# Kernel optimization log

Measured on AMD Instinct MI355X. Metric: run time of the kernel, lower is better.

Reference implementation:

```python
import jax, jax.numpy as jnp
import numpy as np

TOP_K = 48
NUM_RBF = 16
NUM_RBF_SC = 8
MAXREL = 32
EDGE_F = 128
EPS_D = 1e-6
LN_EPS = 1e-5


def gather_nodes(nodes, idx):
    # nodes: [B, L, C], idx: [B, L, K] -> [B, L, K, C]
    return jax.vmap(lambda n, i: n[i])(nodes, idx)


def rbf(D, count):
    # D: [..., ] -> [..., count]; mu in [2, 22], sigma = 20/count
    mu = jnp.linspace(2.0, 22.0, count)
    sigma = (22.0 - 2.0) / count
    return jnp.exp(-(((D[..., None] - mu) / sigma) ** 2))


def layer_norm(x, g, b):
    mu = jnp.mean(x, -1, keepdims=True)
    var = jnp.mean((x - mu) ** 2, -1, keepdims=True)
    return g * (x - mu) / jnp.sqrt(var + LN_EPS) + b


def setup_inputs() -> dict:
    key = jax.random.key(0)
    ks = jax.random.split(key, 8)
    B, Lr = 1, 1024
    X = jax.random.normal(ks[0], (B, Lr, 37, 3), dtype=jnp.float32)
    mask = jnp.ones((B, Lr), dtype=jnp.float32)
    atom_mask = jnp.ones((B, Lr, 37), dtype=jnp.float32)
    residue_idx = jnp.arange(B * Lr, dtype=jnp.int64 if jax.config.jax_enable_x64 else jnp.int32).reshape(B, Lr)
    dihedral_mask = jnp.ones((B, Lr), dtype=jnp.float32)
    chain_labels = jnp.zeros((B, Lr), dtype=jnp.int32)
    W_pos = jax.random.normal(ks[1], (16, 2 * MAXREL + 2), dtype=jnp.float32) * 0.1
    b_pos = jnp.zeros((16,), dtype=jnp.float32)
    W_e = jax.random.normal(ks[2], (EDGE_F, 16 + NUM_RBF * 25), dtype=jnp.float32) * 0.05
    g_e = jnp.ones((EDGE_F,), dtype=jnp.float32)
    be_e = jnp.zeros((EDGE_F,), dtype=jnp.float32)
    W_s = jax.random.normal(ks[3], (EDGE_F, NUM_RBF_SC * 32 * 5), dtype=jnp.float32) * 0.05
    g_s = jnp.ones((EDGE_F,), dtype=jnp.float32)
    b_s = jnp.zeros((EDGE_F,), dtype=jnp.float32)
    return {"X": X, "L": 1024, "mask": mask, "atom_mask": atom_mask,
            "residue_idx": residue_idx, "dihedral_mask": dihedral_mask,
            "chain_labels": chain_labels, "W_pos": W_pos, "b_pos": b_pos,
            "W_e": W_e, "g_e": g_e, "be_e": be_e, "W_s": W_s, "g_s": g_s, "b_s": b_s}


def reference(X, L, mask, atom_mask, residue_idx, dihedral_mask, chain_labels,
              W_pos, b_pos, W_e, g_e, be_e, W_s, g_s, b_s):
    # Virtual Cb from ideal geometry
    b_v = X[:, :, 1, :] - X[:, :, 0, :]
    c_v = X[:, :, 2, :] - X[:, :, 1, :]
    a_v = jnp.cross(b_v, c_v)
    Cb = -0.58273431 * a_v + 0.56802827 * b_v - 0.54067466 * c_v + X[:, :, 1, :]
    Ca = X[:, :, 1, :]
    N = X[:, :, 0, :]
    C = X[:, :, 2, :]
    O = X[:, :, 4, :]

    # _dist: masked pairwise Ca distances + top-k smallest
    mask2d = mask[:, None, :] * mask[:, :, None]  # [B, L, L]
    dX = Ca[:, :, None, :] - Ca[:, None, :, :]
    D = mask2d * jnp.sqrt(jnp.sum(dX ** 2, -1) + EPS_D)
    D_max = jnp.max(D, -1, keepdims=True)
    D_adj = D + (1.0 - mask2d) * D_max
    neg_vals, E_idx = jax.lax.top_k(-D_adj, TOP_K)
    D_neighbors = -neg_vals  # [B, L, K]

    coords = {'N': N, 'Ca': Ca, 'C': C, 'O': O, 'Cb': Cb}
    pairs = [('N','N'),('C','C'),('O','O'),('Cb','Cb'),('Ca','N'),('Ca','C'),('Ca','O'),
             ('Ca','Cb'),('N','C'),('N','O'),('N','Cb'),('Cb','C'),('Cb','O'),('O','C'),
             ('N','Ca'),('C','Ca'),('O','Ca'),('Cb','Ca'),('C','N'),('O','N'),('Cb','N'),
             ('C','Cb'),('O','Cb'),('C','O')]
    A_st = jnp.stack([coords[a] for a, _ in pairs])  # [24, B, L, 3]
    B_st = jnp.stack([coords[b] for _, b in pairs])
    B_nb = jax.vmap(gather_nodes, (0, None))(B_st, E_idx)  # [24, B, L, K, 3]
    Dp = jnp.sqrt(jnp.sum((A_st[:, :, :, None, :] - B_nb) ** 2, -1) + EPS_D)  # [24,B,L,K]
    RBF_pairs = rbf(Dp, NUM_RBF)  # [24, B, L, K, 16]
    Bt, Lr, K = E_idx.shape
    RBF_pairs = jnp.moveaxis(RBF_pairs, 0, 3).reshape(Bt, Lr, K, 24 * NUM_RBF)
    RBF_all = jnp.concatenate([rbf(D_neighbors, NUM_RBF), RBF_pairs], -1)  # [B,L,K,400]

    # Positional encodings
    ri_nb = gather_nodes(residue_idx[..., None], E_idx)[..., 0]  # [B,L,K]
    offset = residue_idx[:, :, None] - ri_nb
    ch_nb = gather_nodes(chain_labels[..., None], E_idx)[..., 0]
    E_chains = (chain_labels[:, :, None] - ch_nb == 0).astype(jnp.int32)
    d = jnp.clip(offset + MAXREL, 0, 2 * MAXREL) * E_chains + (1 - E_chains) * (2 * MAXREL + 1)
    d_onehot = jax.nn.one_hot(d, 2 * MAXREL + 2, dtype=jnp.float32)
    E_positional = d_onehot @ W_pos.T + b_pos
    E = jnp.concatenate([E_positional, RBF_all], -1)  # [B,L,K,416]

    # Sidechain RBFs on the first min(100, K) neighbors
    Ks = min(100, K)
    E_idx_sub = E_idx[:, :, :Ks]
    am_g = gather_nodes(atom_mask, E_idx_sub)  # [B,L,Ks,37]
    S = X[:, :, 5:37, :]  # [B,L,32,3]
    S_nb = gather_nodes(S.reshape(Bt, Lr, 32 * 3), E_idx_sub).reshape(Bt, Lr, Ks, 32, 3)
    anchors = jnp.stack([N, Ca, C, O, Cb], 2)  # [B,L,5,3], anchor order matches loop order
    Ds = jnp.sqrt(jnp.sum((anchors[:, :, None, :, None, :] - S_nb[:, :, :, None, :, :]) ** 2, -1) + EPS_D)
    # Ds: [B,L,Ks,5,32]; rbf_side -> [B,L,Ks,5,32,8]; masked by neighbor atom mask
    RBF_s = rbf(Ds, NUM_RBF_SC) * am_g[:, :, :, None, 5:37, None]
    E_s = RBF_s.reshape(Bt, Lr, Ks, 5 * 32 * NUM_RBF_SC)  # [B,L,Ks,1280]

    E_s = layer_norm(E_s @ W_s.T, g_s, b_s)
    E = layer_norm(E @ W_e.T, g_e, be_e)
    return (E, E_idx, E_s, E_idx_sub)
```

## Files before the change

### kernel.cpp

```cpp
#include <hip/hip_runtime.h>
#include <math.h>

#define LRES 1024
#define TOPK 48
#define NEDGE (LRES*TOPK)

typedef short short8 __attribute__((ext_vector_type(8)));
typedef float f32x4  __attribute__((ext_vector_type(4)));

#define OUT_E     0
#define OUT_EIDX  6291456
#define OUT_ES    6340608
#define OUT_EIDX2 12632064

#define WS_COORDS 0
#define WS_DNB    15360
#define WS_EIDX   64512
#define WS_WPE    113664
#define WS_WPS    140288

#define DE 1.06666667f
#define QE 0.10273976f
#define DS 1.14285714f
#define QS 0.07337053f

__constant__ int PA[24] = {0,2,3,4,1,1,1,1,0,0,0,4,4,3,0,2,3,4,2,3,4,2,3,2};
__constant__ int PB[24] = {0,2,3,4,0,2,3,4,2,3,4,2,3,2,1,1,1,1,0,0,0,4,4,3};

__device__ inline short f2bf(float f) {
    unsigned u = __float_as_uint(f);
    unsigned r = (u + 0x7FFFu + ((u >> 16) & 1u)) >> 16;
    return (short)r;
}

__device__ inline short8 pack8(const float* fv) {
    union { short8 s; unsigned u[4]; } r;
    #pragma unroll
    for (int i = 0; i < 4; ++i)
        r.u[i] = __builtin_amdgcn_perm(__float_as_uint(fv[2*i+1]),
                                       __float_as_uint(fv[2*i]), 0x07060302u);
    return r.s;
}

__global__ __launch_bounds__(256) void k_pre(const float* __restrict__ X,
                                             const float* __restrict__ mask,
                                             const float* __restrict__ We,
                                             const float* __restrict__ Ws,
                                             float* __restrict__ coords,
                                             short* __restrict__ WpE,
                                             short* __restrict__ WpS,
                                             float* __restrict__ Dnb,
                                             int* __restrict__ Eidx,
                                             float* __restrict__ out) {
    int blk = blockIdx.x, t = threadIdx.x;
    if (blk < 256) {
        __shared__ float sCa[LRES*3];
        __shared__ float sM[LRES];
        for (int j = t; j < LRES; j += 256) {
            sCa[j*3+0] = X[j*111 + 3];
            sCa[j*3+1] = X[j*111 + 4];
            sCa[j*3+2] = X[j*111 + 5];
            sM[j] = mask[j];
        }
        __syncthreads();
        int w = t >> 6, lane = t & 63;
        int i = blk * 4 + w;
        float cx = sCa[i*3], cy = sCa[i*3+1], cz = sCa[i*3+2];
        float mi = sM[i];
        float dv[16], m2v[16];
        float lmax = -1e30f;
        #pragma unroll
        for (int s = 0; s < 16; ++s) {
            int j = s*64 + lane;
            float dx = cx - sCa[j*3], dy = cy - sCa[j*3+1], dz = cz - sCa[j*3+2];
            float d  = __builtin_amdgcn_sqrtf(dx*dx + dy*dy + dz*dz + 1e-6f);
            float m2 = mi * sM[j];
            dv[s] = m2 * d; m2v[s] = m2;
            lmax = fmaxf(lmax, dv[s]);
        }
        #pragma unroll
        for (int off = 32; off; off >>= 1) lmax = fmaxf(lmax, __shfl_xor(lmax, off));
        unsigned long long key[16];
        unsigned long long mkey = ~0ull; int mslot = 0;
        #pragma unroll
        for (int s = 0; s < 16; ++s) {
            float dadj = dv[s] + (1.0f - m2v[s]) * lmax;
            key[s] = (((unsigned long long)__float_as_uint(dadj)) << 10) | (unsigned)(s*64 + lane);
            if (key[s] < mkey) { mkey = key[s]; mslot = s; }
        }
        for (int it = 0; it < TOPK; ++it) {
            unsigned long long wk = mkey;
            #pragma unroll
            for (int off = 32; off; off >>= 1) {
                unsigned long long o = __shfl_xor(wk, off);
                wk = (o < wk) ? o : wk;
            }
            if (lane == 0) {
                int j = (int)(wk & 1023u);
                int id = i*TOPK + it;
                Dnb[id]  = __uint_as_float((unsigned)(wk >> 10));
                Eidx[id] = j;
                out[OUT_EIDX  + id] = (float)j;
                out[OUT_EIDX2 + id] = (float)j;
            }
            if (mkey == wk) {
                key[mslot] = ~0ull;
                mkey = ~0ull;
                #pragma unroll
                for (int s = 0; s < 16; ++s)
                    if (key[s] < mkey) { mkey = key[s]; mslot = s; }
            }
        }
    } else if (blk < 896) {
        int g = (blk - 256) * 256 + t;
        if (g < 8*13*64*8) {
            int j = g & 7, lane = (g >> 3) & 63, gg = g >> 9;
            int ks = gg % 13, nt = gg / 13;
            int n = nt*16 + (lane & 15), k = ks*32 + (lane >> 4)*8 + j;
            WpE[g] = f2bf(We[n*416 + k]);
        }
        if (g < 8*40*64*8) {
            int j = g & 7, lane = (g >> 3) & 63, gg = g >> 9;
            int ks = gg % 40, nt = gg / 40;
            int n = nt*16 + (lane & 15), k = ks*32 + (lane >> 4)*8 + j;
            WpS[g] = f2bf(Ws[n*1280 + k]);
        }
    } else {
        int r = (blk - 896) * 256 + t;
        if (r >= LRES) return;
        const float* xr = X + r * 111;
        float N[3], Ca[3], C[3], O[3], bv[3], cv[3], av[3];
        #pragma unroll
        for (int d = 0; d < 3; ++d) {
            N[d]  = xr[0*3 + d];  Ca[d] = xr[1*3 + d];
            C[d]  = xr[2*3 + d];  O[d]  = xr[4*3 + d];
            bv[d] = Ca[d] - N[d]; cv[d] = C[d] - Ca[d];
        }
        av[0] = bv[1]*cv[2] - bv[2]*cv[1];
        av[1] = bv[2]*cv[0] - bv[0]*cv[2];
        av[2] = bv[0]*cv[1] - bv[1]*cv[0];
        float* o = coords + r * 15;
        #pragma unroll
        for (int d = 0; d < 3; ++d) {
            float Cb = -0.58273431f*av[d] + 0.56802827f*bv[d] - 0.54067466f*cv[d] + Ca[d];
            o[0*3+d] = N[d]; o[1*3+d] = Ca[d]; o[2*3+d] = C[d];
            o[3*3+d] = O[d]; o[4*3+d] = Cb;
        }
    }
}

__global__ __launch_bounds__(256, 2) void k_edge(const float* __restrict__ coords,
                                                 const float* __restrict__ X,
                                                 const float* __restrict__ amask,
                                                 const short* __restrict__ WpE,
                                                 const short* __restrict__ WpS,
                                                 const float* __restrict__ Dnb,
                                                 const int* __restrict__ Eidx,
                                                 const int* __restrict__ ri,
                                                 const int* __restrict__ ch,
                                                 const float* __restrict__ Wpos,
                                                 const float* __restrict__ bpos,
                                                 const float* __restrict__ ge,
                                                 const float* __restrict__ be,
                                                 const float* __restrict__ gs,
                                                 const float* __restrict__ bs,
                                                 float* __restrict__ out) {
    __shared__ float smem[5808];
    int t = threadIdx.x;
    int w = t >> 6, lane = t & 63, quad = lane >> 4, l16 = lane & 15;

    if (blockIdx.x < 1536) {
        float* u_hbuf = smem;
        float* sA3    = smem + 4224;
        float* part   = smem + 4272;
        float* part2  = smem + 4528;
        float* smu    = smem + 4784;
        float* srs    = smem + 4816;
        int id0 = blockIdx.x * 32;
        int i0 = id0 / TOPK;

        if (t < 45) {
            int rr = i0 + t / 15;
            if (rr > LRES-1) rr = LRES-1;
            sA3[t] = coords[rr*15 + t%15];
        }
        int s1 = 4*w + quad;
        float S[2][2][3], am[2][2];
        int im[2];
        #pragma unroll
        for (int mt = 0; mt < 2; ++mt) {
            int id = id0 + mt*16 + l16;
            int j  = Eidx[id];
            im[mt] = id / TOPK;
            const float* xp = X + (j*37 + 5)*3;
            const float* ap = amask + j*37 + 5;
            #pragma unroll
            for (int h = 0; h < 2; ++h) {
                int s = s1 + h*16;
                S[mt][h][0] = xp[s*3+0];
                S[mt][h][1] = xp[s*3+1];
                S[mt][h][2] = xp[s*3+2];
                am[mt][h]   = ap[s];
            }
        }
        __syncthreads();

        f32x4 acc[2][8] = {};
        const short8* bp = (const short8*)WpS;

        for (int a = 0; a < 5; ++a) {
            float A[2][3];
            #pragma unroll
            for (int mt = 0; mt < 2; ++mt) {
                int base = (im[mt] - i0)*15 + a*3;
                A[mt][0] = sA3[base+0];
                A[mt][1] = sA3[base+1];
                A[mt][2] = sA3[base+2];
            }
            #pragma unroll
            for (int h = 0; h < 2; ++h) {
                int ks = a*8 + w + h*4;
                short8 afrag[2];
                #pragma unroll
                for (int mt = 0; mt < 2; ++mt) {
                    float dx = A[mt][0] - S[mt][h][0];
                    float dy = A[mt][1] - S[mt][h][1];
                    float dz = A[mt][2] - S[mt][h][2];
                    float d  = __builtin_amdgcn_sqrtf(fmaf(dz,dz,fmaf(dy,dy,fmaf(dx,dx,1e-6f))));
                    float u  = fmaf(d, 0.4f, -0.8f);
                    float e0 = __expf(-u*u) * am[mt][h];
                    float g  = __expf(fmaf(2.0f*DS, u, -DS*DS));
                    float fv[8];
                    fv[0] = e0;
                    #pragma unroll
                    for (int r = 1; r < 8; ++r) { e0 *= g; g *= QS; fv[r] = e0; }
                    afrag[mt] = pack8(fv);
                }
                #pragma unroll
                for (int nt = 0; nt < 8; ++nt) {
                    short8 b = bp[(nt*40 + ks)*64 + lane];
                    acc[0][nt] = __builtin_amdgcn_mfma_f32_16x16x32_bf16(afrag[0], b, acc[0][nt], 0,0,0);
                    acc[1][nt] = __builtin_amdgcn_mfma_f32_16x16x32_bf16(afrag[1], b, acc[1][nt], 0,0,0);
                }
            }
        }

        float* hbuf = u_hbuf;
        __syncthreads();
        for (int ww = 0; ww < 4; ++ww) {
            if (w == ww) {
                #pragma unroll
                for (int mt = 0; mt < 2; ++mt)
                #pragma unroll
                for (int nt = 0; nt < 8; ++nt)
                #pragma unroll
                for (int r = 0; r < 4; ++r) {
                    int e = mt*16 + quad*4 + r;
                    float* p = &hbuf[e*132 + nt*16 + l16];
                    if (ww == 0) *p = acc[mt][nt][r]; else *p += acc[mt][nt][r];
                }
            }
            __syncthreads();
        }
        {
            int e = t >> 3, p = t & 7;
            float s = 0.f, s2 = 0.f;
            #pragma unroll
            for (int q = 0; q < 16; ++q) {
                float x = hbuf[e*132 + p*16 + q];
                s += x; s2 += x*x;
            }
            part[e*8+p] = s; part2[e*8+p] = s2;
        }
        __syncthreads();
        if (t < 32) {
            float s = 0.f, s2 = 0.f;
            #pragma unroll
            for (int p = 0; p < 8; ++p) { s += part[t*8+p]; s2 += part2[t*8+p]; }
            float mu = s * (1.0f/128.0f);
            float var = s2 * (1.0f/128.0f) - mu*mu;
            smu[t] = mu; srs[t] = rsqrtf(var + 1e-5f);
        }
        __syncthreads();
        for (int it = t; it < 32*128; it += 256) {
            int e = it >> 7, f = it & 127;
            float x = hbuf[e*132 + f];
            out[OUT_ES + (size_t)(id0 + e)*128 + f] = gs[f] * (x - smu[e]) * srs[e] + bs[f];
        }
    } else {
        float* sA     = smem;
        float* sB     = smem + 480;
        float* u_hbuf = smem + 960;
        float* part   = smem + 5184;
        float* part2  = smem + 5440;
        float* smu    = smem + 5696;
        float* srs    = smem + 5728;
        int*   sdpos  = (int*)(smem + 5760);
        float* sdist  = u_hbuf;
        float* sposf  = u_hbuf + 32*27;
        int id0 = (blockIdx.x - 1536) * 32;

        if (t < 32) {
            int id = id0 + t, i = id / TOPK, j = Eidx[id];
            int off = ri[i] - ri[j];
            sdpos[t] = (ch[i] == ch[j]) ? min(max(off + 32, 0), 64) : 65;
            sdist[t*27] = Dnb[id];
        }
        for (int it = t; it < 32*15; it += 256) {
            int e = it / 15, q = it % 15;
            int id = id0 + e, i = id / TOPK, j = Eidx[id];
            sA[e*15+q] = coords[i*15+q];
            sB[e*15+q] = coords[j*15+q];
        }
        __syncthreads();
        for (int it = t; it < 32*24; it += 256) {
            int e = it / 24, p = it % 24, a = PA[p], b = PB[p];
            float dx = sA[e*15+a*3+0] - sB[e*15+b*3+0];
            float dy = sA[e*15+a*3+1] - sB[e*15+b*3+1];
            float dz = sA[e*15+a*3+2] - sB[e*15+b*3+2];
            sdist[e*27 + 1 + p] = __builtin_amdgcn_sqrtf(dx*dx + dy*dy + dz*dz + 1e-6f);
        }
        for (int it = t; it < 32*16; it += 256) {
            int e = it >> 4, c = it & 15;
            sposf[e*17 + c] = Wpos[c*66 + sdpos[e]] + bpos[c];
        }
        __syncthreads();

        f32x4 acc[2][8] = {};
        const short8* bp = (const short8*)WpE;
        float rb = (quad & 1) ? 8.0f*DE : 0.0f;

        for (int ks = w; ks < 13; ks += 4) {
            short8 afrag[2];
            #pragma unroll
            for (int mt = 0; mt < 2; ++mt) {
                int e = mt*16 + l16;
                float fv[8];
                if (ks == 0 && quad < 2) {
                    #pragma unroll
                    for (int j = 0; j < 8; ++j) fv[j] = sposf[e*17 + quad*8 + j];
                } else {
                    int p = (ks == 0) ? 0 : (2*ks - 1 + (quad >> 1));
                    float d = sdist[e*27 + p];
                    float u = fmaf(d, 0.8f, -1.6f) - rb;
                    float e0 = __expf(-u*u);
                    float g  = __expf(fmaf(2.0f*DE, u, -DE*DE));
                    fv[0] = e0;
                    #pragma unroll
                    for (int r = 1; r < 8; ++r) { e0 *= g; g *= QE; fv[r] = e0; }
                }
                afrag[mt] = pack8(fv);
            }
            #pragma unroll
            for (int nt = 0; nt < 8; ++nt) {
                short8 b = bp[(nt*13 + ks)*64 + lane];
                acc[0][nt] = __builtin_amdgcn_mfma_f32_16x16x32_bf16(afrag[0], b, acc[0][nt], 0,0,0);
                acc[1][nt] = __builtin_amdgcn_mfma_f32_16x16x32_bf16(afrag[1], b, acc[1][nt], 0,0,0);
            }
        }

        float* hbuf = u_hbuf;
        __syncthreads();
        for (int ww = 0; ww < 4; ++ww) {
            if (w == ww) {
                #pragma unroll
                for (int mt = 0; mt < 2; ++mt)
                #pragma unroll
                for (int nt = 0; nt < 8; ++nt)
                #pragma unroll
                for (int r = 0; r < 4; ++r) {
                    int e = mt*16 + quad*4 + r;
                    float* p = &hbuf[e*132 + nt*16 + l16];
                    if (ww == 0) *p = acc[mt][nt][r]; else *p += acc[mt][nt][r];
                }
            }
            __syncthreads();
        }
        {
            int e = t >> 3, p = t & 7;
            float s = 0.f, s2 = 0.f;
            #pragma unroll
            for (int q = 0; q < 16; ++q) {
                float x = hbuf[e*132 + p*16 + q];
                s += x; s2 += x*x;
            }
            part[e*8+p] = s; part2[e*8+p] = s2;
        }
        __syncthreads();
        if (t < 32) {
            float s = 0.f, s2 = 0.f;
            #pragma unroll
            for (int p = 0; p < 8; ++p) { s += part[t*8+p]; s2 += part2[t*8+p]; }
            float mu = s * (1.0f/128.0f);
            float var = s2 * (1.0f/128.0f) - mu*mu;
            smu[t] = mu; srs[t] = rsqrtf(var + 1e-5f);
        }
        __syncthreads();
        for (int it = t; it < 32*128; it += 256) {
            int e = it >> 7, f = it & 127;
            float x = hbuf[e*132 + f];
            out[OUT_E + (size_t)(id0 + e)*128 + f] = ge[f] * (x - smu[e]) * srs[e] + be[f];
        }
    }
}

extern "C" void kernel_launch(void* const* d_in, const int* in_sizes, int n_in,
                              void* d_out, int out_size, void* d_ws, size_t ws_size,
                              hipStream_t stream) {
    (void)in_sizes; (void)n_in; (void)out_size; (void)ws_size;
    const float* X     = (const float*)d_in[0];
    const float* mask  = (const float*)d_in[2];
    const float* amask = (const float*)d_in[3];
    const int*   ri    = (const int*)d_in[4];
    const int*   ch    = (const int*)d_in[6];
    const float* Wpos  = (const float*)d_in[7];
    const float* bpos  = (const float*)d_in[8];
    const float* We    = (const float*)d_in[9];
    const float* ge    = (const float*)d_in[10];
    const float* be    = (const float*)d_in[11];
    const float* Ws    = (const float*)d_in[12];
    const float* gs    = (const float*)d_in[13];
    const float* bs    = (const float*)d_in[14];

    float* out    = (float*)d_out;
    float* ws     = (float*)d_ws;
    float* coords = ws + WS_COORDS;
    float* Dnb    = ws + WS_DNB;
    int*   Eidx   = (int*)(ws + WS_EIDX);
    short* WpE    = (short*)(ws + WS_WPE);
    short* WpS    = (short*)(ws + WS_WPS);

    k_pre <<<dim3(900),  dim3(256), 0, stream>>>(X, mask, We, Ws, coords,
                                                 WpE, WpS, Dnb, Eidx, out);
    k_edge<<<dim3(3072), dim3(256), 0, stream>>>(coords, X, amask, WpE, WpS,
                                                 Dnb, Eidx, ri, ch, Wpos, bpos,
                                                 ge, be, gs, bs, out);
}
```

Before: 187.6 us.

## Prefetch MFMA weight fragments, interleave edge blocks, vectorize LN stores, branchless top-k

Both edge GEMM loops are fully unrolled and double-buffer the bf16 weight fragments in registers, so the next k-step's loads overlap the current MFMAs. The positional/RBF weight panel is zero-padded from 13 to 16 k-steps to give every wave a uniform trip count, and the workspace offset moves to fit it. Sidechain and backbone blocks are interleaved by block parity rather than split into halves, and occupancy is raised to 3 blocks per SM. The layer-norm epilogues use float4 loads and stores, and the top-k selection uses branchless min/replace instead of slot tracking. The extra prefetch registers may conflict with the higher occupancy target and cause spills.

New measurement: 195.7 us. +4.3%, slower.

```diff
diff --git a/kernel.cpp b/kernel.cpp
--- a/kernel.cpp
+++ b/kernel.cpp
@@ -17,7 +17,7 @@
 #define WS_DNB    15360
 #define WS_EIDX   64512
 #define WS_WPE    113664
-#define WS_WPS    140288
+#define WS_WPS    146432
 
 #define DE 1.06666667f
 #define QE 0.10273976f
@@ -81,13 +81,14 @@
         #pragma unroll
         for (int off = 32; off; off >>= 1) lmax = fmaxf(lmax, __shfl_xor(lmax, off));
         unsigned long long key[16];
-        unsigned long long mkey = ~0ull; int mslot = 0;
         #pragma unroll
         for (int s = 0; s < 16; ++s) {
             float dadj = dv[s] + (1.0f - m2v[s]) * lmax;
             key[s] = (((unsigned long long)__float_as_uint(dadj)) << 10) | (unsigned)(s*64 + lane);
-            if (key[s] < mkey) { mkey = key[s]; mslot = s; }
-        }
+        }
+        unsigned long long mkey = key[0];
+        #pragma unroll
+        for (int s = 1; s < 16; ++s) mkey = (key[s] < mkey) ? key[s] : mkey;
         for (int it = 0; it < TOPK; ++it) {
             unsigned long long wk = mkey;
             #pragma unroll
@@ -104,20 +105,21 @@
                 out[OUT_EIDX2 + id] = (float)j;
             }
             if (mkey == wk) {
-                key[mslot] = ~0ull;
-                mkey = ~0ull;
                 #pragma unroll
                 for (int s = 0; s < 16; ++s)
-                    if (key[s] < mkey) { mkey = key[s]; mslot = s; }
+                    key[s] = (key[s] == wk) ? ~0ull : key[s];
+                mkey = key[0];
+                #pragma unroll
+                for (int s = 1; s < 16; ++s) mkey = (key[s] < mkey) ? key[s] : mkey;
             }
         }
     } else if (blk < 896) {
         int g = (blk - 256) * 256 + t;
-        if (g < 8*13*64*8) {
+        if (g < 8*16*64*8) {
             int j = g & 7, lane = (g >> 3) & 63, gg = g >> 9;
-            int ks = gg % 13, nt = gg / 13;
+            int ks = gg & 15, nt = gg >> 4;
             int n = nt*16 + (lane & 15), k = ks*32 + (lane >> 4)*8 + j;
-            WpE[g] = f2bf(We[n*416 + k]);
+            WpE[g] = (k < 416) ? f2bf(We[n*416 + k]) : (short)0;
         }
         if (g < 8*40*64*8) {
             int j = g & 7, lane = (g >> 3) & 63, gg = g >> 9;
@@ -149,7 +151,7 @@
     }
 }
 
-__global__ __launch_bounds__(256, 2) void k_edge(const float* __restrict__ coords,
+__global__ __launch_bounds__(256, 3) void k_edge(const float* __restrict__ coords,
                                                  const float* __restrict__ X,
                                                  const float* __restrict__ amask,
                                                  const short* __restrict__ WpE,
@@ -168,15 +170,15 @@
     __shared__ float smem[5808];
     int t = threadIdx.x;
     int w = t >> 6, lane = t & 63, quad = lane >> 4, l16 = lane & 15;
-
-    if (blockIdx.x < 1536) {
+    int id0 = (blockIdx.x >> 1) * 32;
+
+    if ((blockIdx.x & 1) == 0) {
         float* u_hbuf = smem;
         float* sA3    = smem + 4224;
         float* part   = smem + 4272;
         float* part2  = smem + 4528;
         float* smu    = smem + 4784;
         float* srs    = smem + 4816;
-        int id0 = blockIdx.x * 32;
         int i0 = id0 / TOPK;
 
         if (t < 45) {
@@ -186,12 +188,12 @@
         }
         int s1 = 4*w + quad;
         float S[2][2][3], am[2][2];
-        int im[2];
+        int bA[2];
         #pragma unroll
         for (int mt = 0; mt < 2; ++mt) {
             int id = id0 + mt*16 + l16;
             int j  = Eidx[id];
-            im[mt] = id / TOPK;
+            bA[mt] = (id / TOPK - i0) * 15;
             const float* xp = X + (j*37 + 5)*3;
             const float* ap = amask + j*37 + 5;
             #pragma unroll
@@ -207,41 +209,41 @@
 
         f32x4 acc[2][8] = {};
         const short8* bp = (const short8*)WpS;
-
-        for (int a = 0; a < 5; ++a) {
-            float A[2][3];
+        short8 bnext[8];
+        #pragma unroll
+        for (int nt = 0; nt < 8; ++nt) bnext[nt] = bp[(nt*40 + w)*64 + lane];
+
+        #pragma unroll
+        for (int st = 0; st < 10; ++st) {
+            int a = st >> 1, h = st & 1;
+            short8 bcur[8];
+            #pragma unroll
+            for (int nt = 0; nt < 8; ++nt) bcur[nt] = bnext[nt];
+            if (st < 9) {
+                int ksn = w + (st + 1)*4;
+                #pragma unroll
+                for (int nt = 0; nt < 8; ++nt) bnext[nt] = bp[(nt*40 + ksn)*64 + lane];
+            }
+            short8 afrag[2];
             #pragma unroll
             for (int mt = 0; mt < 2; ++mt) {
-                int base = (im[mt] - i0)*15 + a*3;
-                A[mt][0] = sA3[base+0];
-                A[mt][1] = sA3[base+1];
-                A[mt][2] = sA3[base+2];
-            }
-            #pragma unroll
-            for (int h = 0; h < 2; ++h) {
-                int ks = a*8 + w + h*4;
-                short8 afrag[2];
-                #pragma unroll
-                for (int mt = 0; mt < 2; ++mt) {
-                    float dx = A[mt][0] - S[mt][h][0];
-                    float dy = A[mt][1] - S[mt][h][1];
-                    float dz = A[mt][2] - S[mt][h][2];
-                    float d  = __builtin_amdgcn_sqrtf(fmaf(dz,dz,fmaf(dy,dy,fmaf(dx,dx,1e-6f))));
-                    float u  = fmaf(d, 0.4f, -0.8f);
-                    float e0 = __expf(-u*u) * am[mt][h];
-                    float g  = __expf(fmaf(2.0f*DS, u, -DS*DS));
-                    float fv[8];
-                    fv[0] = e0;
-                    #pragma unroll
-                    for (int r = 1; r < 8; ++r) { e0 *= g; g *= QS; fv[r] = e0; }
-                    afrag[mt] = pack8(fv);
-                }
-                #pragma unroll
-                for (int nt = 0; nt < 8; ++nt) {
-                    short8 b = bp[(nt*40 + ks)*64 + lane];
-                    acc[0][nt] = __builtin_amdgcn_mfma_f32_16x16x32_bf16(afrag[0], b, acc[0][nt], 0,0,0);
-                    acc[1][nt] = __builtin_amdgcn_mfma_f32_16x16x32_bf16(afrag[1], b, acc[1][nt], 0,0,0);
-                }
+                float dx = sA3[bA[mt] + a*3+0] - S[mt][h][0];
+                float dy = sA3[bA[mt] + a*3+1] - S[mt][h][1];
+                float dz = sA3[bA[mt] + a*3+2] - S[mt][h][2];
+                float d  = __builtin_amdgcn_sqrtf(fmaf(dz,dz,fmaf(dy,dy,fmaf(dx,dx,1e-6f))));
+                float u  = fmaf(d, 0.4f, -0.8f);
+                float e0 = __expf(-u*u) * am[mt][h];
+                float g  = __expf(fmaf(2.0f*DS, u, -(DS*DS)));
+                float fv[8];
+                fv[0] = e0;
+                #pragma unroll
+                for (int r = 1; r < 8; ++r) { e0 *= g; g *= QS; fv[r] = e0; }
+                afrag[mt] = pack8(fv);
+            }
+            #pragma unroll
+            for (int nt = 0; nt < 8; ++nt) {
+                acc[0][nt] = __builtin_amdgcn_mfma_f32_16x16x32_bf16(afrag[0], bcur[nt], acc[0][nt], 0,0,0);
+                acc[1][nt] = __builtin_amdgcn_mfma_f32_16x16x32_bf16(afrag[1], bcur[nt], acc[1][nt], 0,0,0);
             }
         }
 
@@ -282,10 +284,18 @@
             smu[t] = mu; srs[t] = rsqrtf(var + 1e-5f);
         }
         __syncthreads();
-        for (int it = t; it < 32*128; it += 256) {
-            int e = it >> 7, f = it & 127;
-            float x = hbuf[e*132 + f];
-            out[OUT_ES + (size_t)(id0 + e)*128 + f] = gs[f] * (x - smu[e]) * srs[e] + bs[f];
+        for (int it = t; it < 32*32; it += 256) {
+            int e = it >> 5, f = (it & 31)*4;
+            float4 x = *(const float4*)&hbuf[e*132 + f];
+            float4 G = *(const float4*)&gs[f];
+            float4 B = *(const float4*)&bs[f];
+            float mu = smu[e], rs = srs[e];
+            float4 r;
+            r.x = G.x*(x.x - mu)*rs + B.x;
+            r.y = G.y*(x.y - mu)*rs + B.y;
+            r.z = G.z*(x.z - mu)*rs + B.z;
+            r.w = G.w*(x.w - mu)*rs + B.w;
+            *(float4*)&out[OUT_ES + (size_t)(id0 + e)*128 + f] = r;
         }
     } else {
         float* sA     = smem;
@@ -298,7 +308,6 @@
         int*   sdpos  = (int*)(smem + 5760);
         float* sdist  = u_hbuf;
         float* sposf  = u_hbuf + 32*27;
-        int id0 = (blockIdx.x - 1536) * 32;
 
         if (t < 32) {
             int id = id0 + t, i = id / TOPK, j = Eidx[id];
@@ -329,8 +338,21 @@
         f32x4 acc[2][8] = {};
         const short8* bp = (const short8*)WpE;
         float rb = (quad & 1) ? 8.0f*DE : 0.0f;
-
-        for (int ks = w; ks < 13; ks += 4) {
+        short8 bnext[8];
+        #pragma unroll
+        for (int nt = 0; nt < 8; ++nt) bnext[nt] = bp[(nt*16 + w)*64 + lane];
+
+        #pragma unroll
+        for (int st = 0; st < 4; ++st) {
+            int ks = w + st*4;
+            short8 bcur[8];
+            #pragma unroll
+            for (int nt = 0; nt < 8; ++nt) bcur[nt] = bnext[nt];
+            if (st < 3) {
+                int ksn = ks + 4;
+                #pragma unroll
+                for (int nt = 0; nt < 8; ++nt) bnext[nt] = bp[(nt*16 + ksn)*64 + lane];
+            }
             short8 afrag[2];
             #pragma unroll
             for (int mt = 0; mt < 2; ++mt) {
@@ -344,7 +366,7 @@
                     float d = sdist[e*27 + p];
                     float u = fmaf(d, 0.8f, -1.6f) - rb;
                     float e0 = __expf(-u*u);
-                    float g  = __expf(fmaf(2.0f*DE, u, -DE*DE));
+                    float g  = __expf(fmaf(2.0f*DE, u, -(DE*DE)));
                     fv[0] = e0;
                     #pragma unroll
                     for (int r = 1; r < 8; ++r) { e0 *= g; g *= QE; fv[r] = e0; }
@@ -353,9 +375,8 @@
             }
             #pragma unroll
             for (int nt = 0; nt < 8; ++nt) {
-                short8 b = bp[(nt*13 + ks)*64 + lane];
-                acc[0][nt] = __builtin_amdgcn_mfma_f32_16x16x32_bf16(afrag[0], b, acc[0][nt], 0,0,0);
-                acc[1][nt] = __builtin_amdgcn_mfma_f32_16x16x32_bf16(afrag[1], b, acc[1][nt], 0,0,0);
+                acc[0][nt] = __builtin_amdgcn_mfma_f32_16x16x32_bf16(afrag[0], bcur[nt], acc[0][nt], 0,0,0);
+                acc[1][nt] = __builtin_amdgcn_mfma_f32_16x16x32_bf16(afrag[1], bcur[nt], acc[1][nt], 0,0,0);
             }
         }
 
@@ -396,10 +417,18 @@
             smu[t] = mu; srs[t] = rsqrtf(var + 1e-5f);
         }
         __syncthreads();
-        for (int it = t; it < 32*128; it += 256) {
-            int e = it >> 7, f = it & 127;
-            float x = hbuf[e*132 + f];
-            out[OUT_E + (size_t)(id0 + e)*128 + f] = ge[f] * (x - smu[e]) * srs[e] + be[f];
+        for (int it = t; it < 32*32; it += 256) {
+            int e = it >> 5, f = (it & 31)*4;
+            float4 x = *(const float4*)&hbuf[e*132 + f];
+            float4 G = *(const float4*)&ge[f];
+            float4 B = *(const float4*)&be[f];
+            float mu = smu[e], rs = srs[e];
+            float4 r;
+            r.x = G.x*(x.x - mu)*rs + B.x;
+            r.y = G.y*(x.y - mu)*rs + B.y;
+            r.z = G.z*(x.z - mu)*rs + B.z;
+            r.w = G.w*(x.w - mu)*rs + B.w;
+            *(float4*)&out[OUT_E + (size_t)(id0 + e)*128 + f] = r;
         }
     }
 }
```

## Unify epilogue with two-buffer reduction, vectorized stores, padded WpE and branchless top-k

Applied to the files above, without the earlier changes.

Merges the two per-branch epilogues into one shared path. The four-warp serial accumulation into LDS (four barriers) becomes a two-buffer scheme: warps 0/1 write, warps 2/3 add, then the two buffers are summed during the LayerNorm statistics pass. Output stores become float4 and the launch-bounds occupancy hint rises from 2 to 3. The E weight panel is zero-padded from 13 to 16 k-steps so each warp runs the same trip count, at the cost of wasted MFMAs on zeros. The top-k selection replaces slot tracking with branchless min/compare loops. Shared memory grows, which may limit the higher occupancy target.

Measured after the change: 190.8 us. About the same (+1.7%).

```diff
diff --git a/kernel.cpp b/kernel.cpp
--- a/kernel.cpp
+++ b/kernel.cpp
@@ -17,7 +17,7 @@
 #define WS_DNB    15360
 #define WS_EIDX   64512
 #define WS_WPE    113664
-#define WS_WPS    140288
+#define WS_WPS    146432
 
 #define DE 1.06666667f
 #define QE 0.10273976f
@@ -81,13 +81,14 @@
         #pragma unroll
         for (int off = 32; off; off >>= 1) lmax = fmaxf(lmax, __shfl_xor(lmax, off));
         unsigned long long key[16];
-        unsigned long long mkey = ~0ull; int mslot = 0;
         #pragma unroll
         for (int s = 0; s < 16; ++s) {
             float dadj = dv[s] + (1.0f - m2v[s]) * lmax;
             key[s] = (((unsigned long long)__float_as_uint(dadj)) << 10) | (unsigned)(s*64 + lane);
-            if (key[s] < mkey) { mkey = key[s]; mslot = s; }
-        }
+        }
+        unsigned long long mkey = key[0];
+        #pragma unroll
+        for (int s = 1; s < 16; ++s) mkey = (key[s] < mkey) ? key[s] : mkey;
         for (int it = 0; it < TOPK; ++it) {
             unsigned long long wk = mkey;
             #pragma unroll
@@ -104,20 +105,21 @@
                 out[OUT_EIDX2 + id] = (float)j;
             }
             if (mkey == wk) {
-                key[mslot] = ~0ull;
-                mkey = ~0ull;
                 #pragma unroll
                 for (int s = 0; s < 16; ++s)
-                    if (key[s] < mkey) { mkey = key[s]; mslot = s; }
+                    key[s] = (key[s] == wk) ? ~0ull : key[s];
+                mkey = key[0];
+                #pragma unroll
+                for (int s = 1; s < 16; ++s) mkey = (key[s] < mkey) ? key[s] : mkey;
             }
         }
     } else if (blk < 896) {
         int g = (blk - 256) * 256 + t;
-        if (g < 8*13*64*8) {
+        if (g < 8*16*64*8) {
             int j = g & 7, lane = (g >> 3) & 63, gg = g >> 9;
-            int ks = gg % 13, nt = gg / 13;
+            int ks = gg & 15, nt = gg >> 4;
             int n = nt*16 + (lane & 15), k = ks*32 + (lane >> 4)*8 + j;
-            WpE[g] = f2bf(We[n*416 + k]);
+            WpE[g] = (k < 416) ? f2bf(We[n*416 + k]) : (short)0;
         }
         if (g < 8*40*64*8) {
             int j = g & 7, lane = (g >> 3) & 63, gg = g >> 9;
@@ -149,7 +151,7 @@
     }
 }
 
-__global__ __launch_bounds__(256, 2) void k_edge(const float* __restrict__ coords,
+__global__ __launch_bounds__(256, 3) void k_edge(const float* __restrict__ coords,
                                                  const float* __restrict__ X,
                                                  const float* __restrict__ amask,
                                                  const short* __restrict__ WpE,
@@ -165,20 +167,28 @@
                                                  const float* __restrict__ gs,
                                                  const float* __restrict__ bs,
                                                  float* __restrict__ out) {
-    __shared__ float smem[5808];
+    __shared__ float smem[9104];
+    float* Ar    = smem;
+    float* Br    = smem + 4224;
+    float* part  = smem + 8448;
+    float* part2 = smem + 8704;
+    float* smu   = smem + 8960;
+    float* srs   = smem + 8992;
+    int*   sdpos = (int*)(smem + 9024);
+    float* sA3   = smem + 9056;
+
     int t = threadIdx.x;
     int w = t >> 6, lane = t & 63, quad = lane >> 4, l16 = lane & 15;
-
-    if (blockIdx.x < 1536) {
-        float* u_hbuf = smem;
-        float* sA3    = smem + 4224;
-        float* part   = smem + 4272;
-        float* part2  = smem + 4528;
-        float* smu    = smem + 4784;
-        float* srs    = smem + 4816;
-        int id0 = blockIdx.x * 32;
+    bool isS = blockIdx.x < 1536;
+    int id0 = (isS ? blockIdx.x : blockIdx.x - 1536) * 32;
+
+    f32x4 acc[2][8] = {};
+    size_t outBase;
+    const float *gW, *bW;
+
+    if (isS) {
+        outBase = OUT_ES; gW = gs; bW = bs;
         int i0 = id0 / TOPK;
-
         if (t < 45) {
             int rr = i0 + t / 15;
             if (rr > LRES-1) rr = LRES-1;
@@ -186,12 +196,12 @@
         }
         int s1 = 4*w + quad;
         float S[2][2][3], am[2][2];
-        int im[2];
+        int bA[2];
         #pragma unroll
         for (int mt = 0; mt < 2; ++mt) {
             int id = id0 + mt*16 + l16;
             int j  = Eidx[id];
-            im[mt] = id / TOPK;
+            bA[mt] = (id / TOPK - i0) * 15;
             const float* xp = X + (j*37 + 5)*3;
             const float* ap = amask + j*37 + 5;
             #pragma unroll
@@ -205,17 +215,14 @@
         }
         __syncthreads();
 
-        f32x4 acc[2][8] = {};
         const short8* bp = (const short8*)WpS;
-
         for (int a = 0; a < 5; ++a) {
             float A[2][3];
             #pragma unroll
             for (int mt = 0; mt < 2; ++mt) {
-                int base = (im[mt] - i0)*15 + a*3;
-                A[mt][0] = sA3[base+0];
-                A[mt][1] = sA3[base+1];
-                A[mt][2] = sA3[base+2];
+                A[mt][0] = sA3[bA[mt] + a*3+0];
+                A[mt][1] = sA3[bA[mt] + a*3+1];
+                A[mt][2] = sA3[bA[mt] + a*3+2];
             }
             #pragma unroll
             for (int h = 0; h < 2; ++h) {
@@ -229,7 +236,7 @@
                     float d  = __builtin_amdgcn_sqrtf(fmaf(dz,dz,fmaf(dy,dy,fmaf(dx,dx,1e-6f))));
                     float u  = fmaf(d, 0.4f, -0.8f);
                     float e0 = __expf(-u*u) * am[mt][h];
-                    float g  = __expf(fmaf(2.0f*DS, u, -DS*DS));
+                    float g  = __expf(fmaf(2.0f*DS, u, -(DS*DS)));
                     float fv[8];
                     fv[0] = e0;
                     #pragma unroll
@@ -244,61 +251,12 @@
                 }
             }
         }
-
-        float* hbuf = u_hbuf;
-        __syncthreads();
-        for (int ww = 0; ww < 4; ++ww) {
-            if (w == ww) {
-                #pragma unroll
-                for (int mt = 0; mt < 2; ++mt)
-                #pragma unroll
-                for (int nt = 0; nt < 8; ++nt)
-                #pragma unroll
-                for (int r = 0; r < 4; ++r) {
-                    int e = mt*16 + quad*4 + r;
-                    float* p = &hbuf[e*132 + nt*16 + l16];
-                    if (ww == 0) *p = acc[mt][nt][r]; else *p += acc[mt][nt][r];
-                }
-            }
-            __syncthreads();
-        }
-        {
-            int e = t >> 3, p = t & 7;
-            float s = 0.f, s2 = 0.f;
-            #pragma unroll
-            for (int q = 0; q < 16; ++q) {
-                float x = hbuf[e*132 + p*16 + q];
-                s += x; s2 += x*x;
-            }
-            part[e*8+p] = s; part2[e*8+p] = s2;
-        }
-        __syncthreads();
-        if (t < 32) {
-            float s = 0.f, s2 = 0.f;
-            #pragma unroll
-            for (int p = 0; p < 8; ++p) { s += part[t*8+p]; s2 += part2[t*8+p]; }
-            float mu = s * (1.0f/128.0f);
-            float var = s2 * (1.0f/128.0f) - mu*mu;
-            smu[t] = mu; srs[t] = rsqrtf(var + 1e-5f);
-        }
-        __syncthreads();
-        for (int it = t; it < 32*128; it += 256) {
-            int e = it >> 7, f = it & 127;
-            float x = hbuf[e*132 + f];
-            out[OUT_ES + (size_t)(id0 + e)*128 + f] = gs[f] * (x - smu[e]) * srs[e] + bs[f];
-        }
     } else {
-        float* sA     = smem;
-        float* sB     = smem + 480;
-        float* u_hbuf = smem + 960;
-        float* part   = smem + 5184;
-        float* part2  = smem + 5440;
-        float* smu    = smem + 5696;
-        float* srs    = smem + 5728;
-        int*   sdpos  = (int*)(smem + 5760);
-        float* sdist  = u_hbuf;
-        float* sposf  = u_hbuf + 32*27;
-        int id0 = (blockIdx.x - 1536) * 32;
+        outBase = OUT_E; gW = ge; bW = be;
+        float* sdist = Ar;
+        float* sposf = Ar + 900;
+        float* sA    = Br;
+        float* sB    = Br + 480;
 
         if (t < 32) {
             int id = id0 + t, i = id / TOPK, j = Eidx[id];
@@ -326,11 +284,9 @@
         }
         __syncthreads();
 
-        f32x4 acc[2][8] = {};
         const short8* bp = (const short8*)WpE;
         float rb = (quad & 1) ? 8.0f*DE : 0.0f;
-
-        for (int ks = w; ks < 13; ks += 4) {
+        for (int ks = w; ks < 16; ks += 4) {
             short8 afrag[2];
             #pragma unroll
             for (int mt = 0; mt < 2; ++mt) {
@@ -344,7 +300,7 @@
                     float d = sdist[e*27 + p];
                     float u = fmaf(d, 0.8f, -1.6f) - rb;
                     float e0 = __expf(-u*u);
-                    float g  = __expf(fmaf(2.0f*DE, u, -DE*DE));
+                    float g  = __expf(fmaf(2.0f*DE, u, -(DE*DE)));
                     fv[0] = e0;
                     #pragma unroll
                     for (int r = 1; r < 8; ++r) { e0 *= g; g *= QE; fv[r] = e0; }
@@ -353,54 +309,70 @@
             }
             #pragma unroll
             for (int nt = 0; nt < 8; ++nt) {
-                short8 b = bp[(nt*13 + ks)*64 + lane];
+                short8 b = bp[(nt*16 + ks)*64 + lane];
                 acc[0][nt] = __builtin_amdgcn_mfma_f32_16x16x32_bf16(afrag[0], b, acc[0][nt], 0,0,0);
                 acc[1][nt] = __builtin_amdgcn_mfma_f32_16x16x32_bf16(afrag[1], b, acc[1][nt], 0,0,0);
             }
         }
-
-        float* hbuf = u_hbuf;
         __syncthreads();
-        for (int ww = 0; ww < 4; ++ww) {
-            if (w == ww) {
-                #pragma unroll
-                for (int mt = 0; mt < 2; ++mt)
-                #pragma unroll
-                for (int nt = 0; nt < 8; ++nt)
-                #pragma unroll
-                for (int r = 0; r < 4; ++r) {
-                    int e = mt*16 + quad*4 + r;
-                    float* p = &hbuf[e*132 + nt*16 + l16];
-                    if (ww == 0) *p = acc[mt][nt][r]; else *p += acc[mt][nt][r];
-                }
-            }
-            __syncthreads();
-        }
-        {
-            int e = t >> 3, p = t & 7;
-            float s = 0.f, s2 = 0.f;
-            #pragma unroll
-            for (int q = 0; q < 16; ++q) {
-                float x = hbuf[e*132 + p*16 + q];
-                s += x; s2 += x*x;
-            }
-            part[e*8+p] = s; part2[e*8+p] = s2;
-        }
-        __syncthreads();
-        if (t < 32) {
-            float s = 0.f, s2 = 0.f;
-            #pragma unroll
-            for (int p = 0; p < 8; ++p) { s += part[t*8+p]; s2 += part2[t*8+p]; }
-            float mu = s * (1.0f/128.0f);
-            float var = s2 * (1.0f/128.0f) - mu*mu;
-            smu[t] = mu; srs[t] = rsqrtf(var + 1e-5f);
-        }
-        __syncthreads();
-        for (int it = t; it < 32*128; it += 256) {
-            int e = it >> 7, f = it & 127;
-            float x = hbuf[e*132 + f];
-            out[OUT_E + (size_t)(id0 + e)*128 + f] = ge[f] * (x - smu[e]) * srs[e] + be[f];
-        }
+    }
+
+    if (w < 2) {
+        float* R = (w == 0) ? Ar : Br;
+        #pragma unroll
+        for (int mt = 0; mt < 2; ++mt)
+        #pragma unroll
+        for (int nt = 0; nt < 8; ++nt)
+        #pragma unroll
+        for (int r = 0; r < 4; ++r)
+            R[(mt*16 + quad*4 + r)*132 + nt*16 + l16] = acc[mt][nt][r];
+    }
+    __syncthreads();
+    if (w >= 2) {
+        float* R = (w == 2) ? Ar : Br;
+        #pragma unroll
+        for (int mt = 0; mt < 2; ++mt)
+        #pragma unroll
+        for (int nt = 0; nt < 8; ++nt)
+        #pragma unroll
+        for (int r = 0; r < 4; ++r)
+            R[(mt*16 + quad*4 + r)*132 + nt*16 + l16] += acc[mt][nt][r];
+    }
+    __syncthreads();
+    {
+        int e = t >> 3, p = t & 7;
+        float s = 0.f, s2 = 0.f;
+        #pragma unroll
+        for (int q = 0; q < 16; ++q) {
+            int f = q*8 + p;
+            float x = Ar[e*132 + f] + Br[e*132 + f];
+            Ar[e*132 + f] = x;
+            s += x; s2 += x*x;
+        }
+        part[e*8+p] = s; part2[e*8+p] = s2;
+    }
+    __syncthreads();
+    if (t < 32) {
+        float s = 0.f, s2 = 0.f;
+        #pragma unroll
+        for (int p = 0; p < 8; ++p) { s += part[t*8+p]; s2 += part2[t*8+p]; }
+        float mu = s * (1.0f/128.0f);
+        float var = s2 * (1.0f/128.0f) - mu*mu;
+        smu[t] = mu; srs[t] = rsqrtf(var + 1e-5f);
+    }
+    __syncthreads();
+    for (int it = t; it < 32*32; it += 256) {
+        int e = it >> 5, f = (it & 31)*4;
+        float4 x = *(const float4*)&Ar[e*132 + f];
+        float4 G = *(const float4*)&gW[f];
+        float4 B = *(const float4*)&bW[f];
+        float mu = smu[e], rs = srs[e];
+        float4 r;
+        r.x = G.x*(x.x - mu)*rs + B.x;
+        r.y = G.y*(x.y - mu)*rs + B.y;
+        r.z = G.z*(x.z - mu)*rs + B.z;
+        r.w = G.w*(x.w - mu)*rs + B.w;
+        *(float4*)&out[outBase + (size_t)(id0 + e)*128 + f] = r;
     }
 }
 
```
